# Kernel tuning notes

Measured on AMD Instinct MI355X. Metric: run time of the kernel, lower is better.

The kernel has to match this reference:

```python
import jax, jax.numpy as jnp
import numpy as np

N_NODES = 100000
N_EDGES = 3200000
N_GRAPHS = 5000
IN_DIM = 11 + 3  # QM9 num_features + pos
HID = 64


def setup_inputs() -> dict:
    key = jax.random.key(0)
    ks = jax.random.split(key, 12)
    x = jax.random.normal(ks[0], (N_NODES, 11), dtype=jnp.float32)
    pos = jax.random.normal(ks[1], (N_NODES, 3), dtype=jnp.float32)
    edge_index = jax.random.randint(ks[2], (2, N_EDGES), 0, N_NODES, dtype=jnp.int32)
    batch = jnp.sort(jax.random.randint(ks[3], (N_NODES,), 0, N_GRAPHS, dtype=jnp.int32))
    s1 = 1.0 / np.sqrt(IN_DIM)
    s2 = 1.0 / np.sqrt(HID)
    return {
        'x': x,
        'pos': pos,
        'edge_index': edge_index,
        'batch': batch,
        'W1_l': jax.random.uniform(ks[4], (IN_DIM, HID), jnp.float32, -s1, s1),
        'W1_r': jax.random.uniform(ks[5], (IN_DIM, HID), jnp.float32, -s1, s1),
        'b1': jax.random.uniform(ks[6], (HID,), jnp.float32, -s1, s1),
        'W2_l': jax.random.uniform(ks[7], (HID, HID), jnp.float32, -s2, s2),
        'W2_r': jax.random.uniform(ks[8], (HID, HID), jnp.float32, -s2, s2),
        'b2': jax.random.uniform(ks[9], (HID,), jnp.float32, -s2, s2),
        'W_lin': jax.random.uniform(ks[10], (HID, 1), jnp.float32, -s2, s2),
        'b_lin': jax.random.uniform(ks[11], (1,), jnp.float32, -s2, s2),
    }


def _sage_conv(h, src, dst, W_l, W_r, b):
    # mean-aggregate source features at target nodes (PyG SAGEConv default)
    msg = h[src]  # [E, D] gather
    agg = jax.ops.segment_sum(msg, dst, num_segments=N_NODES)
    deg = jax.ops.segment_sum(jnp.ones((src.shape[0],), h.dtype), dst, num_segments=N_NODES)
    agg = agg / jnp.maximum(deg, 1.0)[:, None]
    return agg @ W_l + h @ W_r + b


def reference(x, pos, edge_index, batch, W1_l, W1_r, b1, W2_l, W2_r, b2, W_lin, b_lin):
    h = jnp.concatenate([x, pos], axis=1)  # [N, 14]
    src, dst = edge_index[0], edge_index[1]
    h = jax.nn.relu(_sage_conv(h, src, dst, W1_l, W1_r, b1))
    h = jax.nn.relu(_sage_conv(h, src, dst, W2_l, W2_r, b2))
    # global mean pool over graphs
    pooled = jax.ops.segment_sum(h, batch, num_segments=N_GRAPHS)
    cnt = jax.ops.segment_sum(jnp.ones((N_NODES,), h.dtype), batch, num_segments=N_GRAPHS)
    pooled = pooled / jnp.maximum(cnt, 1.0)[:, None]
    return pooled @ W_lin + b_lin  # [G, 1]
```

## Files before the change

kernel.cpp:

```cpp
#include <hip/hip_runtime.h>
#include <hip/hip_fp16.h>

#define IND 14
#define INDP 16
#define HIDD 64
#define RB 512
#define NB_MAX 256
#define BH_BLOCKS 256
#define CAP 18432
#define ROW1 20
#define DSTS (13 * 1024)

typedef unsigned int uint;
typedef unsigned short ushort;

__device__ __forceinline__ __half2 u2h2(uint u) { return *reinterpret_cast<__half2*>(&u); }

__global__ __launch_bounds__(1024) void bscat_fused(
        const float* __restrict__ x, const float* __restrict__ pos,
        float* __restrict__ h0p, __half* __restrict__ h0h, int N,
        const int* __restrict__ ei, int* __restrict__ gcur,
        uint* __restrict__ pairs, int E, int NB, int chunk) {
    __shared__ int cntS[NB_MAX];
    __shared__ int baseS[NB_MAX];
    __shared__ int dstS[DSTS];
    int tot = N * INDP;
    for (int i = blockIdx.x * 1024 + threadIdx.x; i < tot; i += BH_BLOCKS * 1024) {
        int n = i >> 4, d = i & 15;
        float v = 0.0f;
        if (d < 11) v = x[n * 11 + d];
        else if (d < 14) v = pos[n * 3 + (d - 11)];
        h0p[i] = v;
        h0h[i] = __float2half(v);
    }
    if (threadIdx.x < NB_MAX) cntS[threadIdx.x] = 0;
    __syncthreads();
    int start = blockIdx.x * chunk;
    int end = min(start + chunk, E);
    int it = 0;
    for (int e = start + threadIdx.x; e < end; e += 1024, ++it) {
        int d = ei[E + e];
        dstS[it * 1024 + threadIdx.x] = d;
        atomicAdd(&cntS[d >> 9], 1);
    }
    __syncthreads();
    if (threadIdx.x < NB) {
        int c = cntS[threadIdx.x];
        baseS[threadIdx.x] = c ? atomicAdd(&gcur[threadIdx.x], c) : 0;
        cntS[threadIdx.x] = 0;
    }
    __syncthreads();
    it = 0;
    for (int e = start + threadIdx.x; e < end; e += 1024, ++it) {
        int s = ei[e];
        int d = dstS[it * 1024 + threadIdx.x];
        int b = d >> 9;
        int p = atomicAdd(&cntS[b], 1) + baseS[b];
        pairs[(size_t)b * CAP + p] = ((uint)(d & (RB - 1)) << 17) | (uint)s;
    }
}

__global__ __launch_bounds__(1024) void csr_build(const uint* __restrict__ pairs,
                                                  const int* __restrict__ gcur,
                                                  int2* __restrict__ rowseg,
                                                  int* __restrict__ csr, int N) {
    __shared__ int s[RB];
    __shared__ int fillS[RB];
    __shared__ ushort localS[CAP];
    int b = blockIdx.x;
    int cnt = gcur[b];
    size_t base = (size_t)b * CAP;
    int t = threadIdx.x;
    if (t < RB) { s[t] = 0; fillS[t] = 0; }
    __syncthreads();
    for (int i = t; i < cnt; i += 1024) {
        int local = (int)(pairs[base + i] >> 17);
        localS[i] = (ushort)local;
        atomicAdd(&s[local], 1);
    }
    __syncthreads();
    for (int off = 1; off < RB; off <<= 1) {
        int v = 0;
        if (t < RB && t >= off) v = s[t - off];
        __syncthreads();
        if (t < RB) s[t] += v;
        __syncthreads();
    }
    int node0 = b << 9;
    if (t < RB) {
        int node = node0 + t;
        if (node < N)
            rowseg[node] = make_int2((int)base + (t ? s[t - 1] : 0), (int)base + s[t]);
    }
    __syncthreads();
    for (int i = t; i < cnt; i += 1024) {
        int local = localS[i];
        int src = (int)(pairs[base + i] & 0x1FFFFu);
        int p = atomicAdd(&fillS[local], 1);
        int segbase = local ? s[local - 1] : 0;
        csr[base + segbase + p] = src;
    }
}

__global__ __launch_bounds__(512) void agg_layer1(
        const float* __restrict__ h0p, const __half* __restrict__ h0h,
        const int2* __restrict__ rowseg, const int* __restrict__ csr,
        const float* __restrict__ W_l, const float* __restrict__ W_r,
        const float* __restrict__ b, float* __restrict__ h1f,
        __half* __restrict__ h1h, int N) {
    __shared__ float sWl[IND * HIDD];
    __shared__ float sWr[IND * HIDD];
    __shared__ float sA[8][ROW1];
    __shared__ float sS[8][ROW1];
    for (int i = threadIdx.x; i < IND * HIDD; i += 512) {
        sWl[i] = W_l[i];
        sWr[i] = W_r[i];
    }
    int w = threadIdx.x >> 6, t = threadIdx.x & 63;
    int node = blockIdx.x * 8 + w;
    if (node < N) {
        int2 seg = rowseg[node];
        int beg = seg.x, end = seg.y;
        int s = t >> 1, hf = t & 1;
        __half2 a[4];
#pragma unroll
        for (int j = 0; j < 4; ++j) a[j] = __float2half2_rn(0.0f);
        for (int cb = beg; cb < end; cb += 64) {
            int e0 = cb + s, e1 = e0 + 32;
            int i0 = csr[min(e0, end - 1)];
            int i1 = csr[min(e1, end - 1)];
            __half2 m0 = __float2half2_rn((e0 < end) ? 1.f : 0.f);
            __half2 m1 = __float2half2_rn((e1 < end) ? 1.f : 0.f);
            const uint4 v0 = *(const uint4*)(h0h + (size_t)i0 * INDP + hf * 8);
            const uint4 v1 = *(const uint4*)(h0h + (size_t)i1 * INDP + hf * 8);
            a[0] = __hfma2(u2h2(v0.x), m0, a[0]);
            a[1] = __hfma2(u2h2(v0.y), m0, a[1]);
            a[2] = __hfma2(u2h2(v0.z), m0, a[2]);
            a[3] = __hfma2(u2h2(v0.w), m0, a[3]);
            a[0] = __hfma2(u2h2(v1.x), m1, a[0]);
            a[1] = __hfma2(u2h2(v1.y), m1, a[1]);
            a[2] = __hfma2(u2h2(v1.z), m1, a[2]);
            a[3] = __hfma2(u2h2(v1.w), m1, a[3]);
        }
        float acc[8];
#pragma unroll
        for (int j = 0; j < 4; ++j) {
            float2 f = __half22float2(a[j]);
            acc[2 * j] = f.x;
            acc[2 * j + 1] = f.y;
        }
#pragma unroll
        for (int m = 2; m < 64; m <<= 1) {
#pragma unroll
            for (int j = 0; j < 8; ++j) acc[j] += __shfl_xor(acc[j], m, 64);
        }
        float invd = 1.0f / fmaxf((float)(end - beg), 1.0f);
        if (t < 2) {
#pragma unroll
            for (int j = 0; j < 8; ++j) sA[w][t * 8 + j] = acc[j] * invd;
        }
        if (t < INDP) sS[w][t] = h0p[(size_t)node * INDP + t];
    }
    __syncthreads();
    if (node >= N) return;
    float acc = b[t];
#pragma unroll
    for (int k = 0; k < IND; ++k)
        acc += sA[w][k] * sWl[k * HIDD + t] + sS[w][k] * sWr[k * HIDD + t];
    float val = fmaxf(acc, 0.0f);
    h1f[(size_t)node * HIDD + t] = val;
    h1h[(size_t)node * HIDD + t] = __float2half(val);
}

__global__ __launch_bounds__(512) void agg_layer2(
        const float* __restrict__ h1f, const __half* __restrict__ h1h,
        const int2* __restrict__ rowseg, const int* __restrict__ csr,
        const int* __restrict__ batch,
        const float* __restrict__ W_l, const float* __restrict__ W_r,
        const float* __restrict__ b,
        float* __restrict__ pooled, float* __restrict__ cnt, int N) {
    __shared__ float sA[8][HIDD];
    __shared__ float sS[8][HIDD];
    __shared__ float sP[8][8][HIDD];
    int w = threadIdx.x >> 6, t = threadIdx.x & 63;
    int kb = w * 8;
    int node = blockIdx.x * 8 + w;
    if (node < N) {
        int2 seg = rowseg[node];
        int beg = seg.x, end = seg.y;
        int s = t >> 3, p = t & 7;
        __half2 a[4];
#pragma unroll
        for (int j = 0; j < 4; ++j) a[j] = __float2half2_rn(0.0f);
        for (int cb = beg; cb < end; cb += 32) {
            int e0 = cb + s, e1 = e0 + 8, e2 = e0 + 16, e3 = e0 + 24;
            int i0 = csr[min(e0, end - 1)];
            int i1 = csr[min(e1, end - 1)];
            int i2 = csr[min(e2, end - 1)];
            int i3 = csr[min(e3, end - 1)];
            __half2 m0 = __float2half2_rn((e0 < end) ? 1.f : 0.f);
            __half2 m1 = __float2half2_rn((e1 < end) ? 1.f : 0.f);
            __half2 m2 = __float2half2_rn((e2 < end) ? 1.f : 0.f);
            __half2 m3 = __float2half2_rn((e3 < end) ? 1.f : 0.f);
            const uint4 v0 = *(const uint4*)(h1h + (size_t)i0 * HIDD + p * 8);
            const uint4 v1 = *(const uint4*)(h1h + (size_t)i1 * HIDD + p * 8);
            const uint4 v2 = *(const uint4*)(h1h + (size_t)i2 * HIDD + p * 8);
            const uint4 v3 = *(const uint4*)(h1h + (size_t)i3 * HIDD + p * 8);
            a[0] = __hfma2(u2h2(v0.x), m0, a[0]);
            a[1] = __hfma2(u2h2(v0.y), m0, a[1]);
            a[2] = __hfma2(u2h2(v0.z), m0, a[2]);
            a[3] = __hfma2(u2h2(v0.w), m0, a[3]);
            a[0] = __hfma2(u2h2(v1.x), m1, a[0]);
            a[1] = __hfma2(u2h2(v1.y), m1, a[1]);
            a[2] = __hfma2(u2h2(v1.z), m1, a[2]);
            a[3] = __hfma2(u2h2(v1.w), m1, a[3]);
            a[0] = __hfma2(u2h2(v2.x), m2, a[0]);
            a[1] = __hfma2(u2h2(v2.y), m2, a[1]);
            a[2] = __hfma2(u2h2(v2.z), m2, a[2]);
            a[3] = __hfma2(u2h2(v2.w), m2, a[3]);
            a[0] = __hfma2(u2h2(v3.x), m3, a[0]);
            a[1] = __hfma2(u2h2(v3.y), m3, a[1]);
            a[2] = __hfma2(u2h2(v3.z), m3, a[2]);
            a[3] = __hfma2(u2h2(v3.w), m3, a[3]);
        }
        float acc[8];
#pragma unroll
        for (int j = 0; j < 4; ++j) {
            float2 f = __half22float2(a[j]);
            acc[2 * j] = f.x;
            acc[2 * j + 1] = f.y;
        }
#pragma unroll
        for (int m = 8; m < 64; m <<= 1) {
#pragma unroll
            for (int j = 0; j < 8; ++j) acc[j] += __shfl_xor(acc[j], m, 64);
        }
        float invd = 1.0f / fmaxf((float)(end - beg), 1.0f);
        if (t < 8) {
#pragma unroll
            for (int j = 0; j < 8; ++j) sA[w][t * 8 + j] = acc[j] * invd;
        }
        sS[w][t] = h1f[(size_t)node * HIDD + t];
    }
    float wl[8], wr[8];
#pragma unroll
    for (int kk = 0; kk < 8; ++kk) {
        wl[kk] = W_l[(kb + kk) * HIDD + t];
        wr[kk] = W_r[(kb + kk) * HIDD + t];
    }
    __syncthreads();
#pragma unroll
    for (int n = 0; n < 8; ++n) {
        const float4* pa = (const float4*)(&sA[n][kb]);
        const float4* ps = (const float4*)(&sS[n][kb]);
        float4 a0 = pa[0], a1 = pa[1], s0 = ps[0], s1 = ps[1];
        float acc;
        acc  = a0.x * wl[0] + a0.y * wl[1] + a0.z * wl[2] + a0.w * wl[3];
        acc += a1.x * wl[4] + a1.y * wl[5] + a1.z * wl[6] + a1.w * wl[7];
        acc += s0.x * wr[0] + s0.y * wr[1] + s0.z * wr[2] + s0.w * wr[3];
        acc += s1.x * wr[4] + s1.y * wr[5] + s1.z * wr[6] + s1.w * wr[7];
        sP[w][n][t] = acc;
    }
    __syncthreads();
    if (node >= N) return;
    float v = b[t];
#pragma unroll
    for (int j = 0; j < 8; ++j) v += sP[j][w][t];
    float val = fmaxf(v, 0.0f);
    int g = batch[node];
    atomicAdd(pooled + (size_t)g * HIDD + t, val);
    if (t == 0) atomicAdd(cnt + g, 1.0f);
}

__global__ void final_k(const float* __restrict__ pooled, const float* __restrict__ cnt,
                        const float* __restrict__ W, const float* __restrict__ bl,
                        float* __restrict__ out, int G) {
    int g = blockIdx.x;
    if (g >= G) return;
    int t = threadIdx.x;
    float invc = 1.0f / fmaxf(cnt[g], 1.0f);
    float v = pooled[(size_t)g * HIDD + t] * invc * W[t];
#pragma unroll
    for (int o = 32; o > 0; o >>= 1) v += __shfl_down(v, o, 64);
    if (t == 0) out[g] = v + bl[0];
}

extern "C" void kernel_launch(void* const* d_in, const int* in_sizes, int n_in,
                              void* d_out, int out_size, void* d_ws, size_t ws_size,
                              hipStream_t stream) {
    const float* x   = (const float*)d_in[0];
    const float* pos = (const float*)d_in[1];
    const int* ei    = (const int*)d_in[2];
    const int* batch = (const int*)d_in[3];
    const float* W1l = (const float*)d_in[4];
    const float* W1r = (const float*)d_in[5];
    const float* b1  = (const float*)d_in[6];
    const float* W2l = (const float*)d_in[7];
    const float* W2r = (const float*)d_in[8];
    const float* b2  = (const float*)d_in[9];
    const float* Wl  = (const float*)d_in[10];
    const float* bl  = (const float*)d_in[11];
    float* out = (float*)d_out;

    int N = in_sizes[3];
    int E = in_sizes[2] / 2;
    int G = out_size;
    int NB = (N + RB - 1) >> 9;
    int chunk = (E + BH_BLOCKS - 1) / BH_BLOCKS;

    char* ws = (char*)d_ws;
    size_t off = 0;
    float* cnt = (float*)(ws + off);    off += (size_t)G * 4;
    float* pooled = (float*)(ws + off); off += (size_t)G * HIDD * 4;
    int* gcur = (int*)(ws + off);       off += (size_t)NB_MAX * 4;
    size_t zero_bytes = off;
    off = (off + 255) & ~(size_t)255;
    int2* rowseg = (int2*)(ws + off);   off += (size_t)N * 8;
    uint* pairs = (uint*)(ws + off);    off += (size_t)NB * CAP * 4;
    int* csr    = (int*)(ws + off);     off += (size_t)NB * CAP * 4;
    off = (off + 255) & ~(size_t)255;
    float* h0p  = (float*)(ws + off);   off += (size_t)N * INDP * 4;
    off = (off + 255) & ~(size_t)255;
    __half* h0h = (__half*)(ws + off);  off += (size_t)N * INDP * 2;
    off = (off + 255) & ~(size_t)255;
    float* h1f  = (float*)(ws + off);   off += (size_t)N * HIDD * 4;
    off = (off + 255) & ~(size_t)255;
    __half* h1h = (__half*)(ws + off);  off += (size_t)N * HIDD * 2;

    hipMemsetAsync(d_ws, 0, zero_bytes, stream);

    bscat_fused<<<BH_BLOCKS, 1024, 0, stream>>>(x, pos, h0p, h0h, N,
                                                ei, gcur, pairs, E, NB, chunk);
    csr_build<<<NB, 1024, 0, stream>>>(pairs, gcur, rowseg, csr, N);
    agg_layer1<<<(N + 7) / 8, 512, 0, stream>>>(h0p, h0h, rowseg, csr, W1l, W1r, b1,
                                                h1f, h1h, N);
    agg_layer2<<<(N + 7) / 8, 512, 0, stream>>>(h1f, h1h, rowseg, csr, batch,
                                                W2l, W2r, b2, pooled, cnt, N);
    final_k<<<G, 64, 0, stream>>>(pooled, cnt, Wl, bl, out, G);
}
```

Baseline: 324.8 us.

## Process two nodes per wavefront in layer-2 aggregation with interleaved gathers

Each wavefront in agg_layer2 now aggregates two destination nodes at once, interleaving their CSR index loads and feature gathers to raise memory-level parallelism. The block handles 16 nodes, and the W_l/W_r weight registers are reused for two rounds of the dense transform. This halves the grid size and amortises weight loads, at the cost of more registers, an extra barrier round and divergence when the two nodes' degrees differ.

New measurement: 322.3 us. No clear change (-0.8%).

```diff
diff --git a/kernel.cpp b/kernel.cpp
--- a/kernel.cpp
+++ b/kernel.cpp
@@ -179,68 +179,107 @@
         const float* __restrict__ W_l, const float* __restrict__ W_r,
         const float* __restrict__ b,
         float* __restrict__ pooled, float* __restrict__ cnt, int N) {
-    __shared__ float sA[8][HIDD];
-    __shared__ float sS[8][HIDD];
+    __shared__ float sA[16][HIDD];
+    __shared__ float sS[16][HIDD];
     __shared__ float sP[8][8][HIDD];
     int w = threadIdx.x >> 6, t = threadIdx.x & 63;
     int kb = w * 8;
-    int node = blockIdx.x * 8 + w;
-    if (node < N) {
-        int2 seg = rowseg[node];
-        int beg = seg.x, end = seg.y;
+    int base = blockIdx.x * 16;
+    int nA = base + 2 * w, nB = nA + 1;
+    int begA = 0, endA = 0, begB = 0, endB = 0;
+    if (nA < N) { int2 sg = rowseg[nA]; begA = sg.x; endA = sg.y; }
+    if (nB < N) { int2 sg = rowseg[nB]; begB = sg.x; endB = sg.y; }
+    {
         int s = t >> 3, p = t & 7;
-        __half2 a[4];
-#pragma unroll
-        for (int j = 0; j < 4; ++j) a[j] = __float2half2_rn(0.0f);
-        for (int cb = beg; cb < end; cb += 32) {
-            int e0 = cb + s, e1 = e0 + 8, e2 = e0 + 16, e3 = e0 + 24;
-            int i0 = csr[min(e0, end - 1)];
-            int i1 = csr[min(e1, end - 1)];
-            int i2 = csr[min(e2, end - 1)];
-            int i3 = csr[min(e3, end - 1)];
-            __half2 m0 = __float2half2_rn((e0 < end) ? 1.f : 0.f);
-            __half2 m1 = __float2half2_rn((e1 < end) ? 1.f : 0.f);
-            __half2 m2 = __float2half2_rn((e2 < end) ? 1.f : 0.f);
-            __half2 m3 = __float2half2_rn((e3 < end) ? 1.f : 0.f);
-            const uint4 v0 = *(const uint4*)(h1h + (size_t)i0 * HIDD + p * 8);
-            const uint4 v1 = *(const uint4*)(h1h + (size_t)i1 * HIDD + p * 8);
-            const uint4 v2 = *(const uint4*)(h1h + (size_t)i2 * HIDD + p * 8);
-            const uint4 v3 = *(const uint4*)(h1h + (size_t)i3 * HIDD + p * 8);
-            a[0] = __hfma2(u2h2(v0.x), m0, a[0]);
-            a[1] = __hfma2(u2h2(v0.y), m0, a[1]);
-            a[2] = __hfma2(u2h2(v0.z), m0, a[2]);
-            a[3] = __hfma2(u2h2(v0.w), m0, a[3]);
-            a[0] = __hfma2(u2h2(v1.x), m1, a[0]);
-            a[1] = __hfma2(u2h2(v1.y), m1, a[1]);
-            a[2] = __hfma2(u2h2(v1.z), m1, a[2]);
-            a[3] = __hfma2(u2h2(v1.w), m1, a[3]);
-            a[0] = __hfma2(u2h2(v2.x), m2, a[0]);
-            a[1] = __hfma2(u2h2(v2.y), m2, a[1]);
-            a[2] = __hfma2(u2h2(v2.z), m2, a[2]);
-            a[3] = __hfma2(u2h2(v2.w), m2, a[3]);
-            a[0] = __hfma2(u2h2(v3.x), m3, a[0]);
-            a[1] = __hfma2(u2h2(v3.y), m3, a[1]);
-            a[2] = __hfma2(u2h2(v3.z), m3, a[2]);
-            a[3] = __hfma2(u2h2(v3.w), m3, a[3]);
-        }
-        float acc[8];
+        __half2 aA[4], aB[4];
+#pragma unroll
+        for (int j = 0; j < 4; ++j) { aA[j] = __float2half2_rn(0.f); aB[j] = __float2half2_rn(0.f); }
+        int cbA = begA, cbB = begB;
+        while (cbA < endA || cbB < endB) {
+            bool doA = cbA < endA, doB = cbB < endB;
+            int iA0, iA1, iA2, iA3, iB0, iB1, iB2, iB3;
+            if (doA) {
+                int e0 = cbA + s;
+                iA0 = csr[min(e0, endA - 1)];
+                iA1 = csr[min(e0 + 8, endA - 1)];
+                iA2 = csr[min(e0 + 16, endA - 1)];
+                iA3 = csr[min(e0 + 24, endA - 1)];
+            }
+            if (doB) {
+                int e0 = cbB + s;
+                iB0 = csr[min(e0, endB - 1)];
+                iB1 = csr[min(e0 + 8, endB - 1)];
+                iB2 = csr[min(e0 + 16, endB - 1)];
+                iB3 = csr[min(e0 + 24, endB - 1)];
+            }
+            if (doA) {
+                int e0 = cbA + s;
+                __half2 m0 = __float2half2_rn((e0 < endA) ? 1.f : 0.f);
+                __half2 m1 = __float2half2_rn((e0 + 8 < endA) ? 1.f : 0.f);
+                __half2 m2 = __float2half2_rn((e0 + 16 < endA) ? 1.f : 0.f);
+                __half2 m3 = __float2half2_rn((e0 + 24 < endA) ? 1.f : 0.f);
+                const uint4 v0 = *(const uint4*)(h1h + (size_t)iA0 * HIDD + p * 8);
+                const uint4 v1 = *(const uint4*)(h1h + (size_t)iA1 * HIDD + p * 8);
+                const uint4 v2 = *(const uint4*)(h1h + (size_t)iA2 * HIDD + p * 8);
+                const uint4 v3 = *(const uint4*)(h1h + (size_t)iA3 * HIDD + p * 8);
+                aA[0] = __hfma2(u2h2(v0.x), m0, aA[0]); aA[1] = __hfma2(u2h2(v0.y), m0, aA[1]);
+                aA[2] = __hfma2(u2h2(v0.z), m0, aA[2]); aA[3] = __hfma2(u2h2(v0.w), m0, aA[3]);
+                aA[0] = __hfma2(u2h2(v1.x), m1, aA[0]); aA[1] = __hfma2(u2h2(v1.y), m1, aA[1]);
+                aA[2] = __hfma2(u2h2(v1.z), m1, aA[2]); aA[3] = __hfma2(u2h2(v1.w), m1, aA[3]);
+                aA[0] = __hfma2(u2h2(v2.x), m2, aA[0]); aA[1] = __hfma2(u2h2(v2.y), m2, aA[1]);
+                aA[2] = __hfma2(u2h2(v2.z), m2, aA[2]); aA[3] = __hfma2(u2h2(v2.w), m2, aA[3]);
+                aA[0] = __hfma2(u2h2(v3.x), m3, aA[0]); aA[1] = __hfma2(u2h2(v3.y), m3, aA[1]);
+                aA[2] = __hfma2(u2h2(v3.z), m3, aA[2]); aA[3] = __hfma2(u2h2(v3.w), m3, aA[3]);
+            }
+            if (doB) {
+                int e0 = cbB + s;
+                __half2 m0 = __float2half2_rn((e0 < endB) ? 1.f : 0.f);
+                __half2 m1 = __float2half2_rn((e0 + 8 < endB) ? 1.f : 0.f);
+                __half2 m2 = __float2half2_rn((e0 + 16 < endB) ? 1.f : 0.f);
+                __half2 m3 = __float2half2_rn((e0 + 24 < endB) ? 1.f : 0.f);
+                const uint4 v0 = *(const uint4*)(h1h + (size_t)iB0 * HIDD + p * 8);
+                const uint4 v1 = *(const uint4*)(h1h + (size_t)iB1 * HIDD + p * 8);
+                const uint4 v2 = *(const uint4*)(h1h + (size_t)iB2 * HIDD + p * 8);
+                const uint4 v3 = *(const uint4*)(h1h + (size_t)iB3 * HIDD + p * 8);
+                aB[0] = __hfma2(u2h2(v0.x), m0, aB[0]); aB[1] = __hfma2(u2h2(v0.y), m0, aB[1]);
+                aB[2] = __hfma2(u2h2(v0.z), m0, aB[2]); aB[3] = __hfma2(u2h2(v0.w), m0, aB[3]);
+                aB[0] = __hfma2(u2h2(v1.x), m1, aB[0]); aB[1] = __hfma2(u2h2(v1.y), m1, aB[1]);
+                aB[2] = __hfma2(u2h2(v1.z), m1, aB[2]); aB[3] = __hfma2(u2h2(v1.w), m1, aB[3]);
+                aB[0] = __hfma2(u2h2(v2.x), m2, aB[0]); aB[1] = __hfma2(u2h2(v2.y), m2, aB[1]);
+                aB[2] = __hfma2(u2h2(v2.z), m2, aB[2]); aB[3] = __hfma2(u2h2(v2.w), m2, aB[3]);
+                aB[0] = __hfma2(u2h2(v3.x), m3, aB[0]); aB[1] = __hfma2(u2h2(v3.y), m3, aB[1]);
+                aB[2] = __hfma2(u2h2(v3.z), m3, aB[2]); aB[3] = __hfma2(u2h2(v3.w), m3, aB[3]);
+            }
+            cbA += 32;
+            cbB += 32;
+        }
+        float accA[8], accB[8];
 #pragma unroll
         for (int j = 0; j < 4; ++j) {
-            float2 f = __half22float2(a[j]);
-            acc[2 * j] = f.x;
-            acc[2 * j + 1] = f.y;
+            float2 fA = __half22float2(aA[j]);
+            float2 fB = __half22float2(aB[j]);
+            accA[2 * j] = fA.x; accA[2 * j + 1] = fA.y;
+            accB[2 * j] = fB.x; accB[2 * j + 1] = fB.y;
         }
 #pragma unroll
         for (int m = 8; m < 64; m <<= 1) {
 #pragma unroll
-            for (int j = 0; j < 8; ++j) acc[j] += __shfl_xor(acc[j], m, 64);
-        }
-        float invd = 1.0f / fmaxf((float)(end - beg), 1.0f);
+            for (int j = 0; j < 8; ++j) {
+                accA[j] += __shfl_xor(accA[j], m, 64);
+                accB[j] += __shfl_xor(accB[j], m, 64);
+            }
+        }
+        float invdA = 1.0f / fmaxf((float)(endA - begA), 1.0f);
+        float invdB = 1.0f / fmaxf((float)(endB - begB), 1.0f);
         if (t < 8) {
 #pragma unroll
-            for (int j = 0; j < 8; ++j) sA[w][t * 8 + j] = acc[j] * invd;
-        }
-        sS[w][t] = h1f[(size_t)node * HIDD + t];
+            for (int j = 0; j < 8; ++j) {
+                sA[2 * w][t * 8 + j] = accA[j] * invdA;
+                sA[2 * w + 1][t * 8 + j] = accB[j] * invdB;
+            }
+        }
+        sS[2 * w][t] = (nA < N) ? h1f[(size_t)nA * HIDD + t] : 0.f;
+        sS[2 * w + 1][t] = (nB < N) ? h1f[(size_t)nB * HIDD + t] : 0.f;
     }
     float wl[8], wr[8];
 #pragma unroll
@@ -248,6 +287,7 @@
         wl[kk] = W_l[(kb + kk) * HIDD + t];
         wr[kk] = W_r[(kb + kk) * HIDD + t];
     }
+    float bt = b[t];
     __syncthreads();
 #pragma unroll
     for (int n = 0; n < 8; ++n) {
@@ -262,14 +302,44 @@
         sP[w][n][t] = acc;
     }
     __syncthreads();
-    if (node >= N) return;
-    float v = b[t];
-#pragma unroll
-    for (int j = 0; j < 8; ++j) v += sP[j][w][t];
-    float val = fmaxf(v, 0.0f);
-    int g = batch[node];
-    atomicAdd(pooled + (size_t)g * HIDD + t, val);
-    if (t == 0) atomicAdd(cnt + g, 1.0f);
+    {
+        int nodeE = base + w;
+        if (nodeE < N) {
+            float v = bt;
+#pragma unroll
+            for (int j = 0; j < 8; ++j) v += sP[j][w][t];
+            float val = fmaxf(v, 0.0f);
+            int g = batch[nodeE];
+            atomicAdd(pooled + (size_t)g * HIDD + t, val);
+            if (t == 0) atomicAdd(cnt + g, 1.0f);
+        }
+    }
+    __syncthreads();
+#pragma unroll
+    for (int n = 0; n < 8; ++n) {
+        const float4* pa = (const float4*)(&sA[8 + n][kb]);
+        const float4* ps = (const float4*)(&sS[8 + n][kb]);
+        float4 a0 = pa[0], a1 = pa[1], s0 = ps[0], s1 = ps[1];
+        float acc;
+        acc  = a0.x * wl[0] + a0.y * wl[1] + a0.z * wl[2] + a0.w * wl[3];
+        acc += a1.x * wl[4] + a1.y * wl[5] + a1.z * wl[6] + a1.w * wl[7];
+        acc += s0.x * wr[0] + s0.y * wr[1] + s0.z * wr[2] + s0.w * wr[3];
+        acc += s1.x * wr[4] + s1.y * wr[5] + s1.z * wr[6] + s1.w * wr[7];
+        sP[w][n][t] = acc;
+    }
+    __syncthreads();
+    {
+        int nodeE = base + 8 + w;
+        if (nodeE < N) {
+            float v = bt;
+#pragma unroll
+            for (int j = 0; j < 8; ++j) v += sP[j][w][t];
+            float val = fmaxf(v, 0.0f);
+            int g = batch[nodeE];
+            atomicAdd(pooled + (size_t)g * HIDD + t, val);
+            if (t == 0) atomicAdd(cnt + g, 1.0f);
+        }
+    }
 }
 
 __global__ void final_k(const float* __restrict__ pooled, const float* __restrict__ cnt,
@@ -334,7 +404,7 @@
     csr_build<<<NB, 1024, 0, stream>>>(pairs, gcur, rowseg, csr, N);
     agg_layer1<<<(N + 7) / 8, 512, 0, stream>>>(h0p, h0h, rowseg, csr, W1l, W1r, b1,
                                                 h1f, h1h, N);
-    agg_layer2<<<(N + 7) / 8, 512, 0, stream>>>(h1f, h1h, rowseg, csr, batch,
-                                                W2l, W2r, b2, pooled, cnt, N);
+    agg_layer2<<<(N + 15) / 16, 512, 0, stream>>>(h1f, h1h, rowseg, csr, batch,
+                                                  W2l, W2r, b2, pooled, cnt, N);
     final_k<<<G, 64, 0, stream>>>(pooled, cnt, Wl, bl, out, G);
 }
```
